# Performance work log

Hardware: AMD Instinct MI355X
Metric: run time of the kernel (lower is better)

Reference implementation:

```python
import jax, jax.numpy as jnp
import numpy as np
import math

D_MODEL = 256
D_STATE = 16
D_CONV = 4
EXPAND = 2
N_HEADS = 4
D_INNER = EXPAND * D_MODEL          # 512
DT_RANK = (D_MODEL + 15) // 16      # 16
B_SZ, SEQ = 4, 2048


def setup_inputs() -> dict:
    key = jax.random.key(0)
    ks = jax.random.split(key, 12)
    rn = lambda i, shp, sc=0.02: jax.random.normal(ks[i], shp, dtype=jnp.float32) * sc
    x = jax.random.normal(ks[0], (B_SZ, SEQ, D_MODEL), dtype=jnp.float32)
    return dict(
        x=x,
        ln_g=jnp.ones((D_MODEL,), jnp.float32),
        ln_b=jnp.zeros((D_MODEL,), jnp.float32),
        W_in=rn(1, (D_MODEL, 2 * D_INNER)),
        conv_w=rn(2, (D_INNER, D_CONV), 0.1),
        conv_b=jnp.zeros((D_INNER,), jnp.float32),
        W_xproj=rn(3, (D_INNER, DT_RANK + 2 * D_STATE)),
        W_dt=rn(4, (DT_RANK, D_INNER), 0.1),
        b_dt=jnp.full((D_INNER,), -4.6, jnp.float32),  # softplus ~ 0.01 init
        A_log=jnp.log(jnp.tile(jnp.arange(1, D_STATE + 1, dtype=jnp.float32), (D_INNER, 1))),
        Dp=jnp.ones((D_INNER,), jnp.float32),
        W_out_m=rn(5, (D_INNER, D_MODEL)),
        W_qkv=rn(6, (D_MODEL, 3 * D_MODEL)),
        b_qkv=jnp.zeros((3 * D_MODEL,), jnp.float32),
        W_o=rn(7, (D_MODEL, D_MODEL)),
        b_o=jnp.zeros((D_MODEL,), jnp.float32),
        W_gate=rn(8, (2 * D_MODEL, D_MODEL)),
        b_gate=jnp.zeros((D_MODEL,), jnp.float32),
    )


def _sssd_forward(x, ln_g, ln_b, W_in, conv_w, conv_b, W_xproj, W_dt, b_dt,
                  A_log, Dp, W_out_m, W_qkv, b_qkv, W_o, b_o, W_gate, b_gate):
    B, L, D = x.shape
    # LayerNorm
    mu = x.mean(-1, keepdims=True)
    var = x.var(-1, keepdims=True)
    xn = (x - mu) * jax.lax.rsqrt(var + 1e-5) * ln_g + ln_b

    # ---- Mamba branch ----
    xz = xn @ W_in                      # (B,L,2*D_INNER)
    xm, z = jnp.split(xz, 2, axis=-1)
    # causal depthwise conv1d (kernel D_CONV)
    xp = jnp.pad(xm, ((0, 0), (D_CONV - 1, 0), (0, 0)))
    xc = conv_b + sum(xp[:, k:k + L, :] * conv_w[:, k] for k in range(D_CONV))
    xc = jax.nn.silu(xc)
    dbl = xc @ W_xproj                  # (B,L,DT_RANK+2*D_STATE)
    dt_in = dbl[..., :DT_RANK]
    Bm = dbl[..., DT_RANK:DT_RANK + D_STATE]
    Cm = dbl[..., DT_RANK + D_STATE:]
    dt = jax.nn.softplus(dt_in @ W_dt + b_dt)   # (B,L,D_INNER)
    A = -jnp.exp(A_log)                 # (D_INNER, D_STATE)

    def step(h, inp):
        x_t, dt_t, B_t, C_t = inp       # (B,Din),(B,Din),(B,N),(B,N)
        dA = jnp.exp(dt_t[..., None] * A)               # (B,Din,N)
        h = dA * h + (dt_t * x_t)[..., None] * B_t[:, None, :]
        y = jnp.einsum('bdn,bn->bd', h, C_t)
        return h, y

    h0 = jnp.zeros((B, D_INNER, D_STATE), x.dtype)
    xs = (jnp.swapaxes(xc, 0, 1), jnp.swapaxes(dt, 0, 1),
          jnp.swapaxes(Bm, 0, 1), jnp.swapaxes(Cm, 0, 1))
    _, ys = jax.lax.scan(step, h0, xs)
    y = jnp.swapaxes(ys, 0, 1) + xc * Dp
    y = y * jax.nn.silu(z)
    ssm_out = y @ W_out_m               # (B,L,D)

    # ---- MHSA branch (eval: no dropout) ----
    hd = D // N_HEADS
    qkv = xn @ W_qkv + b_qkv
    q, k, v = jnp.split(qkv, 3, axis=-1)
    sh = lambda t: t.reshape(B, L, N_HEADS, hd).transpose(0, 2, 1, 3)
    q, k, v = sh(q), sh(k), sh(v)
    scores = jnp.einsum('bhqd,bhkd->bhqk', q, k) * (1.0 / math.sqrt(hd))
    attn = jax.nn.softmax(scores, axis=-1)
    o = jnp.einsum('bhqk,bhkd->bhqd', attn, v).transpose(0, 2, 1, 3).reshape(B, L, D)
    attn_out = o @ W_o + b_o

    # ---- sigmoid gate fusion ----
    gate = jax.nn.sigmoid(jnp.concatenate([ssm_out, attn_out], axis=-1) @ W_gate + b_gate)
    fused = gate * ssm_out + (1.0 - gate) * attn_out
    return x + fused


def reference(x, ln_g, ln_b, W_in, conv_w, conv_b, W_xproj, W_dt, b_dt,
              A_log, Dp, W_out_m, W_qkv, b_qkv, W_o, b_o, W_gate, b_gate):
    return _sssd_forward(x, ln_g, ln_b, W_in, conv_w, conv_b, W_xproj, W_dt, b_dt,
                         A_log, Dp, W_out_m, W_qkv, b_qkv, W_o, b_o, W_gate, b_gate)
```

## Files before the change

kernel.cpp:

```cpp
#include <hip/hip_runtime.h>
#include <math.h>

#define B_SZ 4
#define SEQ 2048
#define DM 256
#define DI 512
#define DS 16
#define DTR 16
#define NH 4
#define HD 64
#define T_TOK (B_SZ*SEQ)
#define NCH 64
#define CL (SEQ/NCH)
#define QSCALE 0.18033688f

typedef short bf16x8 __attribute__((ext_vector_type(8)));
typedef float f32x4  __attribute__((ext_vector_type(4)));
typedef unsigned short u16;

__device__ __forceinline__ float sigmoidf_(float x){ return 1.f/(1.f+__expf(-x)); }
__device__ __forceinline__ u16 f2bf(float x){
  unsigned int u = __float_as_uint(x);
  u += 0x7fffu + ((u>>16)&1u);
  return (u16)(u>>16);
}
__device__ __forceinline__ float bf2f(u16 u){ return __uint_as_float(((unsigned)u)<<16); }
__device__ __forceinline__ unsigned cvt_pk_bf16(float lo, float hi){
  unsigned r;
  asm("v_cvt_pk_bf16_f32 %0, %1, %2" : "=v"(r) : "v"(lo), "v"(hi));
  return r;
}

__global__ __launch_bounds__(64) void tcvt_kernel(const float* __restrict__ src,
    u16* __restrict__ dst, int N, int K) {
  int n = blockIdx.x*64 + threadIdx.x;
  int k = blockIdx.y;
  dst[(size_t)n*K + k] = f2bf(src[(size_t)k*N + n]);
}

__global__ __launch_bounds__(64) void tcvt_pad_kernel(const float* __restrict__ src,
    u16* __restrict__ dst, int K, int Nvalid) {
  int n = threadIdx.x;
  int k = blockIdx.y;
  dst[(size_t)n*K + k] = (n < Nvalid) ? f2bf(src[(size_t)k*Nvalid + n]) : (u16)0;
}

__global__ __launch_bounds__(256) void ln_kernel(const float* __restrict__ x,
    const float* __restrict__ g, const float* __restrict__ b,
    u16* __restrict__ xn_bf) {
  int wid = threadIdx.x >> 6;
  int lane = threadIdx.x & 63;
  int token = blockIdx.x*4 + wid;
  const float* xr = x + (size_t)token*DM;
  float4 v = *(const float4*)&xr[lane*4];
  float s  = v.x+v.y+v.z+v.w;
  float ss = v.x*v.x+v.y*v.y+v.z*v.z+v.w*v.w;
  for (int m=1;m<64;m<<=1){ s += __shfl_xor(s,m); ss += __shfl_xor(ss,m); }
  float mu  = s * (1.f/DM);
  float var = ss*(1.f/DM) - mu*mu;
  float rs  = rsqrtf(var + 1e-5f);
  float4 gv = *(const float4*)&g[lane*4];
  float4 bv = *(const float4*)&b[lane*4];
  uint2 o;
  o.x = cvt_pk_bf16((v.x-mu)*rs*gv.x + bv.x, (v.y-mu)*rs*gv.y + bv.y);
  o.y = cvt_pk_bf16((v.z-mu)*rs*gv.z + bv.z, (v.w-mu)*rs*gv.w + bv.w);
  *(uint2*)&xn_bf[(size_t)token*DM + lane*4] = o;
}

template<int ACT>
__global__ __launch_bounds__(256) void gemm_mfma(const u16* __restrict__ A,
    const u16* __restrict__ Wt, const float* __restrict__ bias,
    float* __restrict__ C, u16* __restrict__ Cbf, int K, int ldc, int nvalid,
    int qcols, float qscale, const float* __restrict__ xres,
    const float* __restrict__ cat2) {
  __shared__ u16 lds[12288];
  int tid = threadIdx.x;
  int m0 = blockIdx.y*128, n0 = blockIdx.x*64;
  int w = tid>>6, l = tid&63, lq = l&15, lg = l>>4;
  int wm = w>>1, wn = w&1;
  f32x4 acc[4][2] = {};
  for (int k0 = 0; k0 < K; k0 += 64) {
#pragma unroll
    for (int i=0;i<4;++i){
      int gid = i*256 + tid;
      int row = gid>>3, g = gid&7;
      *(bf16x8*)&lds[row*64 + ((g ^ (row&7))*8)] =
          *(const bf16x8*)&A[(size_t)(m0+row)*K + k0 + g*8];
    }
#pragma unroll
    for (int i=0;i<2;++i){
      int gid = i*256 + tid;
      int row = gid>>3, g = gid&7;
      *(bf16x8*)&lds[8192 + row*64 + ((g ^ (row&7))*8)] =
          *(const bf16x8*)&Wt[(size_t)(n0+row)*K + k0 + g*8];
    }
    __syncthreads();
#pragma unroll
    for (int ks=0;ks<2;++ks){
      bf16x8 af[4], bfv[2];
#pragma unroll
      for (int mi=0;mi<4;++mi){
        int row = wm*64 + mi*16 + lq;
        af[mi] = *(bf16x8*)&lds[row*64 + (((ks*4+lg) ^ (row&7))*8)];
      }
#pragma unroll
      for (int nj=0;nj<2;++nj){
        int row = wn*32 + nj*16 + lq;
        bfv[nj] = *(bf16x8*)&lds[8192 + row*64 + (((ks*4+lg) ^ (row&7))*8)];
      }
#pragma unroll
      for (int mi=0;mi<4;++mi)
#pragma unroll
        for (int nj=0;nj<2;++nj)
          acc[mi][nj] = __builtin_amdgcn_mfma_f32_16x16x32_bf16(af[mi], bfv[nj], acc[mi][nj], 0,0,0);
    }
    __syncthreads();
  }
#pragma unroll
  for (int mi=0;mi<4;++mi){
#pragma unroll
    for (int nj=0;nj<2;++nj){
#pragma unroll
      for (int r=0;r<4;++r){
        int row = m0 + wm*64 + mi*16 + lg*4 + r;
        int col = n0 + wn*32 + nj*16 + lq;
        if (col < nvalid) {
          float v = acc[mi][nj][r];
          if (bias) v += bias[col];
          if (col < qcols) v *= qscale;
          if (ACT==2) {
            float g = sigmoidf_(v);
            float sv = cat2[(size_t)row*512 + col];
            float av = cat2[(size_t)row*512 + 256 + col];
            C[(size_t)row*256 + col] = xres[(size_t)row*256 + col] + g*sv + (1.f-g)*av;
          } else {
            if (ACT==1) v = sigmoidf_(v);
            if (C)   C[(size_t)row*ldc + col] = v;
            if (Cbf) Cbf[(size_t)row*ldc + col] = f2bf(v);
          }
        }
      }
    }
  }
}

__global__ __launch_bounds__(256) void conv_kernel(const u16* __restrict__ xzb,
    const float* __restrict__ cw, const float* __restrict__ cb,
    u16* __restrict__ xc_bf) {
  int idx = blockIdx.x*256 + threadIdx.x;
  int d2 = (idx & 255)*2;
  int t = idx >> 8;
  int l = t & (SEQ-1);
  float acc0 = cb[d2], acc1 = cb[d2+1];
  float4 wA = *(const float4*)&cw[d2*4];
  float4 wB = *(const float4*)&cw[d2*4+4];
  const u16* base = xzb + (size_t)t*1024 + d2;
  ushort2 v;
  if (l>=3){ v = *(const ushort2*)&base[-3*1024]; acc0 += bf2f(v.x)*wA.x; acc1 += bf2f(v.y)*wB.x; }
  if (l>=2){ v = *(const ushort2*)&base[-2*1024]; acc0 += bf2f(v.x)*wA.y; acc1 += bf2f(v.y)*wB.y; }
  if (l>=1){ v = *(const ushort2*)&base[-1*1024]; acc0 += bf2f(v.x)*wA.z; acc1 += bf2f(v.y)*wB.z; }
  v = *(const ushort2*)&base[0];
  acc0 += bf2f(v.x)*wA.w; acc1 += bf2f(v.y)*wB.w;
  float r0 = acc0 * sigmoidf_(acc0);
  float r1 = acc1 * sigmoidf_(acc1);
  *(unsigned*)&xc_bf[(size_t)t*DI + d2] = cvt_pk_bf16(r0, r1);
}

__global__ __launch_bounds__(256) void dt_kernel(const float* __restrict__ dbl,
    const float* __restrict__ Wdt, const float* __restrict__ bdt,
    float* __restrict__ dt) {
  __shared__ float sdbl[4][16];
  int wid = threadIdx.x>>6, lane = threadIdx.x&63;
  int token = blockIdx.x*4 + wid;
  if (lane < 16) sdbl[wid][lane] = dbl[(size_t)token*48 + lane];
  __syncthreads();
  float din[16];
#pragma unroll
  for (int k=0;k<16;++k) din[k] = sdbl[wid][k];
#pragma unroll
  for (int r=0;r<8;++r){
    int d = lane + r*64;
    float acc = bdt[d];
#pragma unroll
    for (int k=0;k<16;++k) acc += din[k]*Wdt[k*DI+d];
    float sp = (acc > 20.f) ? acc : log1pf(__expf(acc));
    dt[(size_t)token*DI+d] = sp;
  }
}

__global__ __launch_bounds__(512) void scan_p1(const u16* __restrict__ xc_bf,
    const float* __restrict__ dt, const float* __restrict__ dbl,
    const float* __restrict__ A_log, float* __restrict__ Pws, float* __restrict__ Hws) {
  __shared__ float sB[CL][16];
  int d = threadIdx.x;
  int bc = blockIdx.x;
  int b = bc >> 6, c = bc & 63;
  {
    int t = threadIdx.x >> 4, n = threadIdx.x & 15;
    sB[t][n] = dbl[((size_t)b*SEQ + c*CL + t)*48 + DTR + n];
  }
  __syncthreads();
  float An[16];
#pragma unroll
  for (int i=0;i<4;++i){
    float4 a = *(const float4*)&A_log[d*16 + i*4];
    An[i*4+0] = -__expf(a.x); An[i*4+1] = -__expf(a.y);
    An[i*4+2] = -__expf(a.z); An[i*4+3] = -__expf(a.w);
  }
  float h[16] = {};
  float P[16];
#pragma unroll
  for (int n=0;n<16;++n) P[n] = 1.f;
  size_t tok = (size_t)b*SEQ + c*CL;
  for (int t=0;t<CL;++t,++tok){
    float dtv = dt[tok*DI+d];
    float xcv = bf2f(xc_bf[tok*DI+d]);
    float u = dtv*xcv;
    float4 B0 = *(float4*)&sB[t][0];
    float4 B1 = *(float4*)&sB[t][4];
    float4 B2 = *(float4*)&sB[t][8];
    float4 B3 = *(float4*)&sB[t][12];
    float Bv[16] = {B0.x,B0.y,B0.z,B0.w,B1.x,B1.y,B1.z,B1.w,
                    B2.x,B2.y,B2.z,B2.w,B3.x,B3.y,B3.z,B3.w};
#pragma unroll
    for (int n=0;n<16;++n){
      float e = __expf(dtv*An[n]);
      P[n] *= e;
      h[n] = e*h[n] + u*Bv[n];
    }
  }
  size_t base = (((size_t)b*NCH + c)*DI + d)*16;
#pragma unroll
  for (int n=0;n<16;++n){ Pws[base+n] = P[n]; Hws[base+n] = h[n]; }
}

__global__ __launch_bounds__(256) void scan_combine(const float* __restrict__ Pws,
    const float* __restrict__ Hws, float* __restrict__ H0ws) {
  int gid = blockIdx.x*256 + threadIdx.x;
  int b  = gid >> 13;
  int dn = gid & 8191;
  float h0 = 0.f;
#pragma unroll 4
  for (int c=0;c<NCH;++c){
    size_t idx = ((size_t)(b*NCH+c)<<13) + dn;
    H0ws[idx] = h0;
    h0 = Pws[idx]*h0 + Hws[idx];
  }
}

__global__ __launch_bounds__(512) void scan_p2(const u16* __restrict__ xc_bf,
    const float* __restrict__ dt, const float* __restrict__ dbl,
    const float* __restrict__ A_log, const float* __restrict__ Dp,
    const u16* __restrict__ xzb, const float* __restrict__ H0ws,
    u16* __restrict__ ygate_bf) {
  __shared__ float sBC[CL][32];
  int d = threadIdx.x;
  int bc = blockIdx.x;
  int b = bc >> 6, c = bc & 63;
#pragma unroll
  for (int i=0;i<2;++i){
    int idx = i*512 + threadIdx.x;
    int t = idx >> 5, q = idx & 31;
    sBC[t][q] = dbl[((size_t)b*SEQ + c*CL + t)*48 + DTR + q];
  }
  __syncthreads();
  float An[16];
#pragma unroll
  for (int i=0;i<4;++i){
    float4 a = *(const float4*)&A_log[d*16 + i*4];
    An[i*4+0] = -__expf(a.x); An[i*4+1] = -__expf(a.y);
    An[i*4+2] = -__expf(a.z); An[i*4+3] = -__expf(a.w);
  }
  float Dd = Dp[d];
  float h[16];
  size_t base = (((size_t)b*NCH + c)*DI + d)*16;
#pragma unroll
  for (int i=0;i<4;++i){
    float4 h4 = *(const float4*)&H0ws[base + i*4];
    h[i*4+0]=h4.x; h[i*4+1]=h4.y; h[i*4+2]=h4.z; h[i*4+3]=h4.w;
  }
  size_t tok = (size_t)b*SEQ + c*CL;
  for (int t=0;t<CL;++t,++tok){
    float dtv = dt[tok*DI+d];
    float xcv = bf2f(xc_bf[tok*DI+d]);
    float zv  = bf2f(xzb[tok*1024 + DI + d]);
    float u = dtv*xcv;
    float4 B0 = *(float4*)&sBC[t][0];
    float4 B1 = *(float4*)&sBC[t][4];
    float4 B2 = *(float4*)&sBC[t][8];
    float4 B3 = *(float4*)&sBC[t][12];
    float4 C0 = *(float4*)&sBC[t][16];
    float4 C1 = *(float4*)&sBC[t][20];
    float4 C2 = *(float4*)&sBC[t][24];
    float4 C3 = *(float4*)&sBC[t][28];
    float Bv[16] = {B0.x,B0.y,B0.z,B0.w,B1.x,B1.y,B1.z,B1.w,
                    B2.x,B2.y,B2.z,B2.w,B3.x,B3.y,B3.z,B3.w};
    float Cv[16] = {C0.x,C0.y,C0.z,C0.w,C1.x,C1.y,C1.z,C1.w,
                    C2.x,C2.y,C2.z,C2.w,C3.x,C3.y,C3.z,C3.w};
    float y = 0.f;
#pragma unroll
    for (int n=0;n<16;++n){
      float e = __expf(dtv*An[n]);
      h[n] = e*h[n] + u*Bv[n];
      y += h[n]*Cv[n];
    }
    y += xcv*Dd;
    ygate_bf[tok*DI + d] = f2bf(y * (zv*sigmoidf_(zv)));
  }
}

__global__ __launch_bounds__(256) void vt_kernel(const u16* __restrict__ qkvb,
    u16* __restrict__ vT) {
  int bh = blockIdx.y; int b = bh>>2, h = bh&3;
  int l0 = blockIdx.x*64;
  int d = threadIdx.x & 63;
  int oct = threadIdx.x >> 6;
  u16 tmp[16];
#pragma unroll
  for (int i=0;i<16;++i){
    int l = l0 + oct*16 + i;
    tmp[i] = qkvb[((size_t)b*SEQ + l)*768 + 512 + h*HD + d];
  }
  size_t dst = ((size_t)bh*HD + d)*SEQ + l0 + oct*16;
  *(bf16x8*)&vT[dst]   = *(bf16x8*)&tmp[0];
  *(bf16x8*)&vT[dst+8] = *(bf16x8*)&tmp[8];
}

__global__ __launch_bounds__(256) void attn_mfma_kernel(const u16* __restrict__ qkvb,
    const u16* __restrict__ vT,
    float* __restrict__ Opart, float* __restrict__ ml) {
  __shared__ u16 lds[12288];
  int H = blockIdx.x + 32*blockIdx.y + 512*(int)blockIdx.z;
  int cx = H & 7, k = H >> 3;
  int xq = k & 31;
  int G  = cx*8 + (k >> 5);
  int bh = G & 15, s = G >> 4;
  int b = bh>>2, h = bh&3;
  int tid = threadIdx.x;
  int w = tid>>6, l = tid&63;
  int lq = l & 15;
  int lg = l >> 4;
  size_t bbase = (size_t)b*SEQ;
  size_t vbase = (size_t)bh*HD*SEQ;
  int q0 = xq*64 + w*16;

  bf16x8 qf[2];
#pragma unroll
  for (int dsl=0; dsl<2; ++dsl)
    qf[dsl] = *(const bf16x8*)&qkvb[(bbase + q0 + lq)*768 + h*HD + lg*8 + dsl*32];

  float m_ = -1e30f, l_ = 0.f;
  f32x4 oacc[4] = {{0,0,0,0},{0,0,0,0},{0,0,0,0},{0,0,0,0}};
  int pbase = 8192 + w*1024;

  for (int kt=s*8; kt<s*8+8; ++kt){
    __syncthreads();
#pragma unroll
    for (int i=0;i<2;++i){
      int gid = i*256 + tid;
      int row = gid>>3, g = gid&7;
      *(bf16x8*)&lds[row*64 + ((g ^ (row&7))*8)] =
          *(const bf16x8*)&qkvb[(bbase + kt*64 + row)*768 + 256 + h*HD + g*8];
    }
#pragma unroll
    for (int i=0;i<2;++i){
      int gid = i*256 + tid;
      int row = gid>>3, g = gid&7;
      *(bf16x8*)&lds[4096 + row*64 + ((g ^ (row&7))*8)] =
          *(const bf16x8*)&vT[vbase + (size_t)row*SEQ + kt*64 + g*8];
    }
    __syncthreads();

    f32x4 sacc[4] = {{0,0,0,0},{0,0,0,0},{0,0,0,0},{0,0,0,0}};
    __builtin_amdgcn_s_setprio(1);
#pragma unroll
    for (int kg=0;kg<4;++kg){
#pragma unroll
      for (int dsl=0;dsl<2;++dsl){
        int row = kg*16 + lq;
        bf16x8 kf = *(bf16x8*)&lds[row*64 + (((dsl*4 + lg) ^ (row&7))*8)];
        sacc[kg] = __builtin_amdgcn_mfma_f32_16x16x32_bf16(kf, qf[dsl], sacc[kg], 0,0,0);
      }
    }
    __builtin_amdgcn_s_setprio(0);

    float tm = sacc[0][0];
#pragma unroll
    for (int kg=0;kg<4;++kg){
      float a = fmaxf(fmaxf(sacc[kg][0],sacc[kg][1]),fmaxf(sacc[kg][2],sacc[kg][3]));
      tm = fmaxf(tm, a);
    }
    tm = fmaxf(tm, __shfl_xor(tm,16));
    tm = fmaxf(tm, __shfl_xor(tm,32));
    if (__any(tm - m_ > 8.f)) {
      float mn = fmaxf(m_, tm);
      float sc = exp2f(m_ - mn);
      m_ = mn;
      l_ *= sc;
#pragma unroll
      for (int dg=0;dg<4;++dg){
        oacc[dg][0]*=sc; oacc[dg][1]*=sc; oacc[dg][2]*=sc; oacc[dg][3]*=sc;
      }
    }
    float p[4][4];
    float ps = 0.f;
#pragma unroll
    for (int kg=0;kg<4;++kg)
#pragma unroll
      for (int r=0;r<4;++r){
        float pe = exp2f(sacc[kg][r] - m_);
        p[kg][r] = pe;
        ps += pe;
      }
    ps += __shfl_xor(ps,16);
    ps += __shfl_xor(ps,32);
    l_ += ps;

#pragma unroll
    for (int kg=0;kg<4;++kg)
#pragma unroll
      for (int rp=0;rp<2;++rp){
        unsigned pk = cvt_pk_bf16(p[kg][2*rp], p[kg][2*rp+1]);
        int off = pbase + lq*64 + (((2*kg + (lg>>1)) ^ (lq&7))*8) + 4*(lg&1) + 2*rp;
        *(unsigned*)&lds[off] = pk;
      }

    __builtin_amdgcn_s_setprio(1);
#pragma unroll
    for (int ks=0;ks<2;++ks){
      bf16x8 pf = *(bf16x8*)&lds[pbase + lq*64 + (((ks*4 + lg) ^ (lq&7))*8)];
#pragma unroll
      for (int dg=0;dg<4;++dg){
        int row = dg*16 + lq;
        bf16x8 vf = *(bf16x8*)&lds[4096 + row*64 + (((ks*4 + lg) ^ (row&7))*8)];
        oacc[dg] = __builtin_amdgcn_mfma_f32_16x16x32_bf16(vf, pf, oacc[dg], 0,0,0);
      }
    }
    __builtin_amdgcn_s_setprio(0);
  }

  int sidx = bh*4 + s;
  size_t rb = ((size_t)sidx*SEQ + q0 + lq)*64;
#pragma unroll
  for (int dg=0;dg<4;++dg)
#pragma unroll
    for (int r=0;r<4;++r)
      Opart[rb + dg*16 + lg*4 + r] = oacc[dg][r];
  if (lg==0){
    ml[((size_t)sidx*SEQ + q0 + lq)*2    ] = m_;
    ml[((size_t)sidx*SEQ + q0 + lq)*2 + 1] = l_;
  }
}

__global__ __launch_bounds__(256) void attn_merge_kernel(const float* __restrict__ Opart,
    const float* __restrict__ ml, u16* __restrict__ attn_bf) {
  int w = threadIdx.x>>6, lane = threadIdx.x&63;
  int R = blockIdx.x*4 + w;
  int bh = R>>11, q = R&2047;
  float m[4], lv[4];
#pragma unroll
  for (int s=0;s<4;++s){
    m[s]  = ml[((size_t)(bh*4+s)*SEQ + q)*2];
    lv[s] = ml[((size_t)(bh*4+s)*SEQ + q)*2 + 1];
  }
  float ms = fmaxf(fmaxf(m[0],m[1]),fmaxf(m[2],m[3]));
  float o = 0.f, lsum = 0.f;
#pragma unroll
  for (int s=0;s<4;++s){
    float wsc = exp2f(m[s]-ms);
    lsum += wsc*lv[s];
    o += wsc*Opart[((size_t)(bh*4+s)*SEQ + q)*64 + lane];
  }
  size_t token = (size_t)(bh>>2)*SEQ + q;
  attn_bf[token*DM + (bh&3)*HD + lane] = f2bf(o/lsum);
}

extern "C" void kernel_launch(void* const* d_in, const int* in_sizes, int n_in,
                              void* d_out, int out_size, void* d_ws, size_t ws_size,
                              hipStream_t stream) {
  const float* x      = (const float*)d_in[0];
  const float* ln_g   = (const float*)d_in[1];
  const float* ln_b   = (const float*)d_in[2];
  const float* W_in   = (const float*)d_in[3];
  const float* conv_w = (const float*)d_in[4];
  const float* conv_b = (const float*)d_in[5];
  const float* W_xproj= (const float*)d_in[6];
  const float* W_dt   = (const float*)d_in[7];
  const float* b_dt   = (const float*)d_in[8];
  const float* A_log  = (const float*)d_in[9];
  const float* Dp     = (const float*)d_in[10];
  const float* W_out_m= (const float*)d_in[11];
  const float* W_qkv  = (const float*)d_in[12];
  const float* b_qkv  = (const float*)d_in[13];
  const float* W_o    = (const float*)d_in[14];
  const float* b_o    = (const float*)d_in[15];
  const float* W_gate = (const float*)d_in[16];
  const float* b_gate = (const float*)d_in[17];
  float* out = (float*)d_out;

  float* ws = (float*)d_ws;
  u16*   xn_bf   = (u16*)(ws);
  u16*   xzb     = (u16*)(ws + 1048576);
  u16*   qkv_bf  = (u16*)(ws + 9437184);
  u16*   xc_bf   = (u16*)(ws + 12582912);
  float* dblb    = ws + 16777216;
  float* dtb     = ws + 17170432;
  u16*   ygate_bf= (u16*)(ws + 21364736);
  u16*   attn_bf = (u16*)(ws + 23461888);
  float* catb    = ws + 24510464;
  u16*   catb_bf = (u16*)(ws + 28704768);
  float* gateb   = ws + 30801920;
  u16*   Wt_all  = (u16*)(ws + 32899072);
  float* Opart = ws + 1048576;
  float* mlb   = (float*)xn_bf;
  u16*   vTb   = (u16*)dtb;
  float* Pws   = catb;
  float* Hws   = catb + 2097152;
  float* H0ws  = catb + 4194304;
  (void)gateb;

  u16* Wt_in   = Wt_all;
  u16* Wt_qkv  = Wt_all + 262144;
  u16* Wt_out  = Wt_all + 458752;
  u16* Wt_o    = Wt_all + 589824;
  u16* Wt_gate = Wt_all + 655360;
  u16* Wt_xp   = Wt_all + 786432;

  tcvt_kernel<<<dim3(16,256), 64, 0, stream>>>(W_in,    Wt_in,   1024, 256);
  tcvt_kernel<<<dim3(12,256), 64, 0, stream>>>(W_qkv,   Wt_qkv,   768, 256);
  tcvt_kernel<<<dim3(4,512),  64, 0, stream>>>(W_out_m, Wt_out,   256, 512);
  tcvt_kernel<<<dim3(4,256),  64, 0, stream>>>(W_o,     Wt_o,     256, 256);
  tcvt_kernel<<<dim3(4,512),  64, 0, stream>>>(W_gate,  Wt_gate,  256, 512);
  tcvt_pad_kernel<<<dim3(1,512), 64, 0, stream>>>(W_xproj, Wt_xp, 512, 48);

  ln_kernel<<<T_TOK/4, 256, 0, stream>>>(x, ln_g, ln_b, xn_bf);
  gemm_mfma<0><<<dim3(16,64), 256, 0, stream>>>(xn_bf, Wt_in, nullptr, nullptr, xzb, 256, 1024, 1024, 0, 1.f, nullptr, nullptr);
  gemm_mfma<0><<<dim3(12,64), 256, 0, stream>>>(xn_bf, Wt_qkv, b_qkv, nullptr, qkv_bf, 256, 768, 768, 256, QSCALE, nullptr, nullptr);
  conv_kernel<<<T_TOK, 256, 0, stream>>>(xzb, conv_w, conv_b, xc_bf);
  gemm_mfma<0><<<dim3(1,64), 256, 0, stream>>>(xc_bf, Wt_xp, nullptr, dblb, nullptr, 512, 48, 48, 0, 1.f, nullptr, nullptr);
  dt_kernel<<<T_TOK/4, 256, 0, stream>>>(dblb, W_dt, b_dt, dtb);
  scan_p1<<<B_SZ*NCH, 512, 0, stream>>>(xc_bf, dtb, dblb, A_log, Pws, Hws);
  scan_combine<<<128, 256, 0, stream>>>(Pws, Hws, H0ws);
  scan_p2<<<B_SZ*NCH, 512, 0, stream>>>(xc_bf, dtb, dblb, A_log, Dp, xzb, H0ws, ygate_bf);
  vt_kernel<<<dim3(SEQ/64, 16), 256, 0, stream>>>(qkv_bf, vTb);
  attn_mfma_kernel<<<dim3(SEQ/64, 16, 4), 256, 0, stream>>>(qkv_bf, vTb, Opart, mlb);
  attn_merge_kernel<<<8192, 256, 0, stream>>>(Opart, mlb, attn_bf);
  gemm_mfma<0><<<dim3(4,64), 256, 0, stream>>>(ygate_bf, Wt_out, nullptr, catb, catb_bf, 512, 512, 256, 0, 1.f, nullptr, nullptr);
  gemm_mfma<0><<<dim3(4,64), 256, 0, stream>>>(attn_bf, Wt_o, b_o, catb+256, catb_bf+256, 256, 512, 256, 0, 1.f, nullptr, nullptr);
  gemm_mfma<2><<<dim3(4,64), 256, 0, stream>>>(catb_bf, Wt_gate, b_gate, out, nullptr, 512, 256, 256, 0, 1.f, x, catb);
}
```

Baseline: 260.3 us.

## Fuse weight conversions, fold V transpose into QKV GEMM, double-buffer attention

Six per-weight transpose-convert launches become one batched kernel that transposes through an LDS tile. The separate V-transpose kernel is removed; the QKV GEMM epilogue now also writes V transposed, into a workspace slot that no longer aliases dtb. The attention kernel now handles 32 queries per wave (two MFMA query groups) in a 128-query block, which halves the block count and doubles K/V reuse. It also double-buffers K/V tiles in LDS, prefetching the next tile into registers while computing the current one. The costs are higher register and LDS use, lower occupancy, and scattered 2-byte stores in the GEMM epilogue.

```diff
diff --git a/kernel.cpp b/kernel.cpp
--- a/kernel.cpp
+++ b/kernel.cpp
@@ -31,18 +31,34 @@
   return r;
 }
 
-__global__ __launch_bounds__(64) void tcvt_kernel(const float* __restrict__ src,
-    u16* __restrict__ dst, int N, int K) {
-  int n = blockIdx.x*64 + threadIdx.x;
-  int k = blockIdx.y;
-  dst[(size_t)n*K + k] = f2bf(src[(size_t)k*N + n]);
-}
-
-__global__ __launch_bounds__(64) void tcvt_pad_kernel(const float* __restrict__ src,
-    u16* __restrict__ dst, int K, int Nvalid) {
-  int n = threadIdx.x;
-  int k = blockIdx.y;
-  dst[(size_t)n*K + k] = (n < Nvalid) ? f2bf(src[(size_t)k*Nvalid + n]) : (u16)0;
+struct TcvtArgs {
+  const float* src[6];
+  u16* dst[6];
+  int K[6];
+  int Nvalid[6];
+  int Npad[6];
+};
+__global__ __launch_bounds__(256) void tcvt_all(TcvtArgs a) {
+  int wi = blockIdx.z;
+  int K = a.K[wi], Nv = a.Nvalid[wi], Np = a.Npad[wi];
+  int k0 = blockIdx.x*64, n0 = blockIdx.y*64;
+  if (k0 >= K || n0 >= Np) return;
+  __shared__ u16 tile[64][65];
+  const float* src = a.src[wi];
+  u16* dst = a.dst[wi];
+  int tn = threadIdx.x & 63, tq = threadIdx.x >> 6;
+#pragma unroll
+  for (int j=0;j<16;++j){
+    int kk = j*4 + tq;
+    int n = n0 + tn;
+    tile[tn][kk] = (n < Nv) ? f2bf(src[(size_t)(k0+kk)*Nv + n]) : (u16)0;
+  }
+  __syncthreads();
+#pragma unroll
+  for (int j=0;j<16;++j){
+    int nn = j*4 + tq;
+    dst[(size_t)(n0+nn)*K + k0 + tn] = tile[nn][tn];
+  }
 }
 
 __global__ __launch_bounds__(256) void ln_kernel(const float* __restrict__ x,
@@ -72,7 +88,7 @@
     const u16* __restrict__ Wt, const float* __restrict__ bias,
     float* __restrict__ C, u16* __restrict__ Cbf, int K, int ldc, int nvalid,
     int qcols, float qscale, const float* __restrict__ xres,
-    const float* __restrict__ cat2) {
+    const float* __restrict__ cat2, u16* __restrict__ vTout) {
   __shared__ u16 lds[12288];
   int tid = threadIdx.x;
   int m0 = blockIdx.y*128, n0 = blockIdx.x*64;
@@ -133,6 +149,13 @@
             float sv = cat2[(size_t)row*512 + col];
             float av = cat2[(size_t)row*512 + 256 + col];
             C[(size_t)row*256 + col] = xres[(size_t)row*256 + col] + g*sv + (1.f-g)*av;
+          } else if (ACT==3) {
+            Cbf[(size_t)row*ldc + col] = f2bf(v);
+            if (col >= 512) {
+              int bb = row>>11, ll = row&2047;
+              int hh = (col-512)>>6, dd = (col-512)&63;
+              vTout[(((size_t)(bb*4+hh))*64 + dd)*SEQ + ll] = f2bf(v);
+            }
           } else {
             if (ACT==1) v = sigmoidf_(v);
             if (C)   C[(size_t)row*ldc + col] = v;
@@ -309,31 +332,14 @@
   }
 }
 
-__global__ __launch_bounds__(256) void vt_kernel(const u16* __restrict__ qkvb,
-    u16* __restrict__ vT) {
-  int bh = blockIdx.y; int b = bh>>2, h = bh&3;
-  int l0 = blockIdx.x*64;
-  int d = threadIdx.x & 63;
-  int oct = threadIdx.x >> 6;
-  u16 tmp[16];
-#pragma unroll
-  for (int i=0;i<16;++i){
-    int l = l0 + oct*16 + i;
-    tmp[i] = qkvb[((size_t)b*SEQ + l)*768 + 512 + h*HD + d];
-  }
-  size_t dst = ((size_t)bh*HD + d)*SEQ + l0 + oct*16;
-  *(bf16x8*)&vT[dst]   = *(bf16x8*)&tmp[0];
-  *(bf16x8*)&vT[dst+8] = *(bf16x8*)&tmp[8];
-}
-
 __global__ __launch_bounds__(256) void attn_mfma_kernel(const u16* __restrict__ qkvb,
     const u16* __restrict__ vT,
     float* __restrict__ Opart, float* __restrict__ ml) {
-  __shared__ u16 lds[12288];
-  int H = blockIdx.x + 32*blockIdx.y + 512*(int)blockIdx.z;
+  __shared__ u16 lds[24576];
+  int H = blockIdx.x + 16*blockIdx.y + 256*(int)blockIdx.z;
   int cx = H & 7, k = H >> 3;
-  int xq = k & 31;
-  int G  = cx*8 + (k >> 5);
+  int xq = k & 15;
+  int G  = cx*8 + (k >> 4);
   int bh = G & 15, s = G >> 4;
   int b = bh>>2, h = bh&3;
   int tid = threadIdx.x;
@@ -342,113 +348,130 @@
   int lg = l >> 4;
   size_t bbase = (size_t)b*SEQ;
   size_t vbase = (size_t)bh*HD*SEQ;
-  int q0 = xq*64 + w*16;
-
-  bf16x8 qf[2];
-#pragma unroll
-  for (int dsl=0; dsl<2; ++dsl)
-    qf[dsl] = *(const bf16x8*)&qkvb[(bbase + q0 + lq)*768 + h*HD + lg*8 + dsl*32];
-
-  float m_ = -1e30f, l_ = 0.f;
-  f32x4 oacc[4] = {{0,0,0,0},{0,0,0,0},{0,0,0,0},{0,0,0,0}};
-  int pbase = 8192 + w*1024;
-
-  for (int kt=s*8; kt<s*8+8; ++kt){
-    __syncthreads();
-#pragma unroll
-    for (int i=0;i<2;++i){
-      int gid = i*256 + tid;
-      int row = gid>>3, g = gid&7;
-      *(bf16x8*)&lds[row*64 + ((g ^ (row&7))*8)] =
-          *(const bf16x8*)&qkvb[(bbase + kt*64 + row)*768 + 256 + h*HD + g*8];
-    }
-#pragma unroll
-    for (int i=0;i<2;++i){
-      int gid = i*256 + tid;
-      int row = gid>>3, g = gid&7;
-      *(bf16x8*)&lds[4096 + row*64 + ((g ^ (row&7))*8)] =
-          *(const bf16x8*)&vT[vbase + (size_t)row*SEQ + kt*64 + g*8];
-    }
-    __syncthreads();
-
-    f32x4 sacc[4] = {{0,0,0,0},{0,0,0,0},{0,0,0,0},{0,0,0,0}};
+  int q0 = xq*128 + w*32;
+
+  bf16x8 qf[2][2];
+#pragma unroll
+  for (int qg=0; qg<2; ++qg)
+#pragma unroll
+    for (int dsl=0; dsl<2; ++dsl)
+      qf[qg][dsl] = *(const bf16x8*)&qkvb[(bbase + q0 + qg*16 + lq)*768 + h*HD + lg*8 + dsl*32];
+
+  float m_[2] = {-1e30f,-1e30f}, l_[2] = {0.f,0.f};
+  f32x4 oacc[2][4] = {};
+  int pbase = 16384 + w*2048;
+
+  int srow = tid>>3, sg = tid&7;
+  int kt0 = s*8;
+  bf16x8 kreg[2], vreg[2];
+
+#define LOADT(kt) { \
+  kreg[0] = *(const bf16x8*)&qkvb[(bbase + (size_t)(kt)*64 + srow)*768 + 256 + h*HD + sg*8]; \
+  kreg[1] = *(const bf16x8*)&qkvb[(bbase + (size_t)(kt)*64 + srow + 32)*768 + 256 + h*HD + sg*8]; \
+  vreg[0] = *(const bf16x8*)&vT[vbase + (size_t)srow*SEQ + (kt)*64 + sg*8]; \
+  vreg[1] = *(const bf16x8*)&vT[vbase + (size_t)(srow+32)*SEQ + (kt)*64 + sg*8]; }
+#define STORET(bi) { \
+  *(bf16x8*)&lds[(bi)*4096 + srow*64 + ((sg ^ (srow&7))*8)] = kreg[0]; \
+  *(bf16x8*)&lds[(bi)*4096 + (srow+32)*64 + ((sg ^ ((srow+32)&7))*8)] = kreg[1]; \
+  *(bf16x8*)&lds[8192 + (bi)*4096 + srow*64 + ((sg ^ (srow&7))*8)] = vreg[0]; \
+  *(bf16x8*)&lds[8192 + (bi)*4096 + (srow+32)*64 + ((sg ^ ((srow+32)&7))*8)] = vreg[1]; }
+
+  LOADT(kt0);
+  STORET(0);
+  __syncthreads();
+  int cur = 0;
+
+  for (int it=0; it<8; ++it){
+    if (it < 7) LOADT(kt0+it+1);
+
+    int kb = cur*4096, vb = 8192 + cur*4096;
+    f32x4 sacc[2][4] = {};
     __builtin_amdgcn_s_setprio(1);
 #pragma unroll
     for (int kg=0;kg<4;++kg){
 #pragma unroll
       for (int dsl=0;dsl<2;++dsl){
         int row = kg*16 + lq;
-        bf16x8 kf = *(bf16x8*)&lds[row*64 + (((dsl*4 + lg) ^ (row&7))*8)];
-        sacc[kg] = __builtin_amdgcn_mfma_f32_16x16x32_bf16(kf, qf[dsl], sacc[kg], 0,0,0);
+        bf16x8 kf = *(bf16x8*)&lds[kb + row*64 + (((dsl*4 + lg) ^ (row&7))*8)];
+        sacc[0][kg] = __builtin_amdgcn_mfma_f32_16x16x32_bf16(kf, qf[0][dsl], sacc[0][kg], 0,0,0);
+        sacc[1][kg] = __builtin_amdgcn_mfma_f32_16x16x32_bf16(kf, qf[1][dsl], sacc[1][kg], 0,0,0);
       }
     }
     __builtin_amdgcn_s_setprio(0);
 
-    float tm = sacc[0][0];
-#pragma unroll
-    for (int kg=0;kg<4;++kg){
-      float a = fmaxf(fmaxf(sacc[kg][0],sacc[kg][1]),fmaxf(sacc[kg][2],sacc[kg][3]));
-      tm = fmaxf(tm, a);
-    }
-    tm = fmaxf(tm, __shfl_xor(tm,16));
-    tm = fmaxf(tm, __shfl_xor(tm,32));
-    if (__any(tm - m_ > 8.f)) {
-      float mn = fmaxf(m_, tm);
-      float sc = exp2f(m_ - mn);
-      m_ = mn;
-      l_ *= sc;
-#pragma unroll
-      for (int dg=0;dg<4;++dg){
-        oacc[dg][0]*=sc; oacc[dg][1]*=sc; oacc[dg][2]*=sc; oacc[dg][3]*=sc;
-      }
-    }
-    float p[4][4];
-    float ps = 0.f;
-#pragma unroll
-    for (int kg=0;kg<4;++kg)
-#pragma unroll
-      for (int r=0;r<4;++r){
-        float pe = exp2f(sacc[kg][r] - m_);
-        p[kg][r] = pe;
-        ps += pe;
-      }
-    ps += __shfl_xor(ps,16);
-    ps += __shfl_xor(ps,32);
-    l_ += ps;
-
-#pragma unroll
-    for (int kg=0;kg<4;++kg)
-#pragma unroll
-      for (int rp=0;rp<2;++rp){
-        unsigned pk = cvt_pk_bf16(p[kg][2*rp], p[kg][2*rp+1]);
-        int off = pbase + lq*64 + (((2*kg + (lg>>1)) ^ (lq&7))*8) + 4*(lg&1) + 2*rp;
-        *(unsigned*)&lds[off] = pk;
-      }
+#pragma unroll
+    for (int qg=0;qg<2;++qg){
+      float tm = sacc[qg][0][0];
+#pragma unroll
+      for (int kg=0;kg<4;++kg){
+        float a = fmaxf(fmaxf(sacc[qg][kg][0],sacc[qg][kg][1]),
+                        fmaxf(sacc[qg][kg][2],sacc[qg][kg][3]));
+        tm = fmaxf(tm, a);
+      }
+      tm = fmaxf(tm, __shfl_xor(tm,16));
+      tm = fmaxf(tm, __shfl_xor(tm,32));
+      if (__any(tm - m_[qg] > 8.f)) {
+        float mn = fmaxf(m_[qg], tm);
+        float sc = exp2f(m_[qg] - mn);
+        m_[qg] = mn;
+        l_[qg] *= sc;
+#pragma unroll
+        for (int dg=0;dg<4;++dg){
+          oacc[qg][dg][0]*=sc; oacc[qg][dg][1]*=sc; oacc[qg][dg][2]*=sc; oacc[qg][dg][3]*=sc;
+        }
+      }
+      float ps = 0.f;
+#pragma unroll
+      for (int kg=0;kg<4;++kg){
+        float p0 = exp2f(sacc[qg][kg][0] - m_[qg]);
+        float p1 = exp2f(sacc[qg][kg][1] - m_[qg]);
+        float p2 = exp2f(sacc[qg][kg][2] - m_[qg]);
+        float p3 = exp2f(sacc[qg][kg][3] - m_[qg]);
+        ps += (p0+p1)+(p2+p3);
+        int off = pbase + qg*1024 + lq*64 + (((2*kg + (lg>>1)) ^ (lq&7))*8) + 4*(lg&1);
+        *(unsigned*)&lds[off]   = cvt_pk_bf16(p0, p1);
+        *(unsigned*)&lds[off+2] = cvt_pk_bf16(p2, p3);
+      }
+      ps += __shfl_xor(ps,16);
+      ps += __shfl_xor(ps,32);
+      l_[qg] += ps;
+    }
 
     __builtin_amdgcn_s_setprio(1);
 #pragma unroll
     for (int ks=0;ks<2;++ks){
-      bf16x8 pf = *(bf16x8*)&lds[pbase + lq*64 + (((ks*4 + lg) ^ (lq&7))*8)];
+      bf16x8 pf0 = *(bf16x8*)&lds[pbase        + lq*64 + (((ks*4 + lg) ^ (lq&7))*8)];
+      bf16x8 pf1 = *(bf16x8*)&lds[pbase + 1024 + lq*64 + (((ks*4 + lg) ^ (lq&7))*8)];
 #pragma unroll
       for (int dg=0;dg<4;++dg){
         int row = dg*16 + lq;
-        bf16x8 vf = *(bf16x8*)&lds[4096 + row*64 + (((ks*4 + lg) ^ (row&7))*8)];
-        oacc[dg] = __builtin_amdgcn_mfma_f32_16x16x32_bf16(vf, pf, oacc[dg], 0,0,0);
+        bf16x8 vf = *(bf16x8*)&lds[vb + row*64 + (((ks*4 + lg) ^ (row&7))*8)];
+        oacc[0][dg] = __builtin_amdgcn_mfma_f32_16x16x32_bf16(vf, pf0, oacc[0][dg], 0,0,0);
+        oacc[1][dg] = __builtin_amdgcn_mfma_f32_16x16x32_bf16(vf, pf1, oacc[1][dg], 0,0,0);
       }
     }
     __builtin_amdgcn_s_setprio(0);
-  }
+
+    if (it < 7) STORET(cur^1);
+    __syncthreads();
+    cur ^= 1;
+  }
+#undef LOADT
+#undef STORET
 
   int sidx = bh*4 + s;
-  size_t rb = ((size_t)sidx*SEQ + q0 + lq)*64;
-#pragma unroll
-  for (int dg=0;dg<4;++dg)
-#pragma unroll
-    for (int r=0;r<4;++r)
-      Opart[rb + dg*16 + lg*4 + r] = oacc[dg][r];
-  if (lg==0){
-    ml[((size_t)sidx*SEQ + q0 + lq)*2    ] = m_;
-    ml[((size_t)sidx*SEQ + q0 + lq)*2 + 1] = l_;
+#pragma unroll
+  for (int qg=0;qg<2;++qg){
+    size_t rb = ((size_t)sidx*SEQ + q0 + qg*16 + lq)*64;
+#pragma unroll
+    for (int dg=0;dg<4;++dg)
+#pragma unroll
+      for (int r=0;r<4;++r)
+        Opart[rb + dg*16 + lg*4 + r] = oacc[qg][dg][r];
+    if (lg==0){
+      ml[((size_t)sidx*SEQ + q0 + qg*16 + lq)*2    ] = m_[qg];
+      ml[((size_t)sidx*SEQ + q0 + qg*16 + lq)*2 + 1] = l_[qg];
+    }
   }
 }
 
@@ -513,11 +536,10 @@
   u16*   Wt_all  = (u16*)(ws + 32899072);
   float* Opart = ws + 1048576;
   float* mlb   = (float*)xn_bf;
-  u16*   vTb   = (u16*)dtb;
+  u16*   vTb   = (u16*)gateb;
   float* Pws   = catb;
   float* Hws   = catb + 2097152;
   float* H0ws  = catb + 4194304;
-  (void)gateb;
 
   u16* Wt_in   = Wt_all;
   u16* Wt_qkv  = Wt_all + 262144;
@@ -526,26 +548,27 @@
   u16* Wt_gate = Wt_all + 655360;
   u16* Wt_xp   = Wt_all + 786432;
 
-  tcvt_kernel<<<dim3(16,256), 64, 0, stream>>>(W_in,    Wt_in,   1024, 256);
-  tcvt_kernel<<<dim3(12,256), 64, 0, stream>>>(W_qkv,   Wt_qkv,   768, 256);
-  tcvt_kernel<<<dim3(4,512),  64, 0, stream>>>(W_out_m, Wt_out,   256, 512);
-  tcvt_kernel<<<dim3(4,256),  64, 0, stream>>>(W_o,     Wt_o,     256, 256);
-  tcvt_kernel<<<dim3(4,512),  64, 0, stream>>>(W_gate,  Wt_gate,  256, 512);
-  tcvt_pad_kernel<<<dim3(1,512), 64, 0, stream>>>(W_xproj, Wt_xp, 512, 48);
+  TcvtArgs ta;
+  ta.src[0]=W_in;    ta.dst[0]=Wt_in;   ta.K[0]=256; ta.Nvalid[0]=1024; ta.Npad[0]=1024;
+  ta.src[1]=W_qkv;   ta.dst[1]=Wt_qkv;  ta.K[1]=256; ta.Nvalid[1]=768;  ta.Npad[1]=768;
+  ta.src[2]=W_out_m; ta.dst[2]=Wt_out;  ta.K[2]=512; ta.Nvalid[2]=256;  ta.Npad[2]=256;
+  ta.src[3]=W_o;     ta.dst[3]=Wt_o;    ta.K[3]=256; ta.Nvalid[3]=256;  ta.Npad[3]=256;
+  ta.src[4]=W_gate;  ta.dst[4]=Wt_gate; ta.K[4]=512; ta.Nvalid[4]=256;  ta.Npad[4]=256;
+  ta.src[5]=W_xproj; ta.dst[5]=Wt_xp;   ta.K[5]=512; ta.Nvalid[5]=48;   ta.Npad[5]=64;
+  tcvt_all<<<dim3(8,16,6), 256, 0, stream>>>(ta);
 
   ln_kernel<<<T_TOK/4, 256, 0, stream>>>(x, ln_g, ln_b, xn_bf);
-  gemm_mfma<0><<<dim3(16,64), 256, 0, stream>>>(xn_bf, Wt_in, nullptr, nullptr, xzb, 256, 1024, 1024, 0, 1.f, nullptr, nullptr);
-  gemm_mfma<0><<<dim3(12,64), 256, 0, stream>>>(xn_bf, Wt_qkv, b_qkv, nullptr, qkv_bf, 256, 768, 768, 256, QSCALE, nullptr, nullptr);
+  gemm_mfma<0><<<dim3(16,64), 256, 0, stream>>>(xn_bf, Wt_in, nullptr, nullptr, xzb, 256, 1024, 1024, 0, 1.f, nullptr, nullptr, nullptr);
+  gemm_mfma<3><<<dim3(12,64), 256, 0, stream>>>(xn_bf, Wt_qkv, b_qkv, nullptr, qkv_bf, 256, 768, 768, 256, QSCALE, nullptr, nullptr, vTb);
   conv_kernel<<<T_TOK, 256, 0, stream>>>(xzb, conv_w, conv_b, xc_bf);
-  gemm_mfma<0><<<dim3(1,64), 256, 0, stream>>>(xc_bf, Wt_xp, nullptr, dblb, nullptr, 512, 48, 48, 0, 1.f, nullptr, nullptr);
+  gemm_mfma<0><<<dim3(1,64), 256, 0, stream>>>(xc_bf, Wt_xp, nullptr, dblb, nullptr, 512, 48, 48, 0, 1.f, nullptr, nullptr, nullptr);
   dt_kernel<<<T_TOK/4, 256, 0, stream>>>(dblb, W_dt, b_dt, dtb);
   scan_p1<<<B_SZ*NCH, 512, 0, stream>>>(xc_bf, dtb, dblb, A_log, Pws, Hws);
   scan_combine<<<128, 256, 0, stream>>>(Pws, Hws, H0ws);
   scan_p2<<<B_SZ*NCH, 512, 0, stream>>>(xc_bf, dtb, dblb, A_log, Dp, xzb, H0ws, ygate_bf);
-  vt_kernel<<<dim3(SEQ/64, 16), 256, 0, stream>>>(qkv_bf, vTb);
-  attn_mfma_kernel<<<dim3(SEQ/64, 16, 4), 256, 0, stream>>>(qkv_bf, vTb, Opart, mlb);
+  attn_mfma_kernel<<<dim3(16, 16, 4), 256, 0, stream>>>(qkv_bf, vTb, Opart, mlb);
   attn_merge_kernel<<<8192, 256, 0, stream>>>(Opart, mlb, attn_bf);
-  gemm_mfma<0><<<dim3(4,64), 256, 0, stream>>>(ygate_bf, Wt_out, nullptr, catb, catb_bf, 512, 512, 256, 0, 1.f, nullptr, nullptr);
-  gemm_mfma<0><<<dim3(4,64), 256, 0, stream>>>(attn_bf, Wt_o, b_o, catb+256, catb_bf+256, 256, 512, 256, 0, 1.f, nullptr, nullptr);
-  gemm_mfma<2><<<dim3(4,64), 256, 0, stream>>>(catb_bf, Wt_gate, b_gate, out, nullptr, 512, 256, 256, 0, 1.f, x, catb);
-}
+  gemm_mfma<0><<<dim3(4,64), 256, 0, stream>>>(ygate_bf, Wt_out, nullptr, catb, catb_bf, 512, 512, 256, 0, 1.f, nullptr, nullptr, nullptr);
+  gemm_mfma<0><<<dim3(4,64), 256, 0, stream>>>(attn_bf, Wt_o, b_o, catb+256, catb_bf+256, 256, 512, 256, 0, 1.f, nullptr, nullptr, nullptr);
+  gemm_mfma<2><<<dim3(4,64), 256, 0, stream>>>(catb_bf, Wt_gate, b_gate, out, nullptr, 512, 256, 256, 0, 1.f, x, catb, nullptr);
+}
```

Measured after the change: 252.5 us. 3.0% less time.
